# Kernel optimization log

Hardware: AMD Instinct MI355X
Metric: run time of the kernel (lower is better)

## Reference

```python
import jax, jax.numpy as jnp
import numpy as np

N_NODES = 100000
N_EDGES = 600000
D = 128
N_CLASSES = 16


def _degrees(idx, n):
    ones = jnp.ones(idx.shape[0], dtype=jnp.float32)
    return jax.ops.segment_sum(ones, idx, num_segments=n)


def graph_conv(src, dst, h, W, b):
    # DGL GraphConv, norm='both': D_out^{-1/2} A D_in^{-1/2} h W + b
    n = h.shape[0]
    deg_out = jnp.maximum(_degrees(src, n), 1.0)
    deg_in = jnp.maximum(_degrees(dst, n), 1.0)
    h = h * jax.lax.rsqrt(deg_out)[:, None]          # src-side norm
    h = h @ W                                         # dense transform
    msg = h[src]                                      # gather  [E, d]
    agg = jax.ops.segment_sum(msg, dst, num_segments=n)  # scatter-add
    agg = agg * jax.lax.rsqrt(deg_in)[:, None]        # dst-side norm
    return agg + b


def setup_inputs() -> dict:
    key = jax.random.key(0)
    ks = jax.random.split(key, 8)
    h = jax.random.normal(ks[0], (N_NODES, D), dtype=jnp.float32)
    src = jax.random.randint(ks[1], (N_EDGES,), 0, N_NODES)
    dst = jax.random.randint(ks[2], (N_EDGES,), 0, N_NODES)
    s = 1.0 / np.sqrt(D)
    W1 = jax.random.normal(ks[3], (D, D), dtype=jnp.float32) * s
    b1 = jnp.zeros((D,), dtype=jnp.float32)
    W2 = jax.random.normal(ks[4], (D, D), dtype=jnp.float32) * s
    b2 = jnp.zeros((D,), dtype=jnp.float32)
    Wc = jax.random.normal(ks[5], (D, N_CLASSES), dtype=jnp.float32) * s
    bc = jnp.zeros((N_CLASSES,), dtype=jnp.float32)
    return {"h": h, "src": src, "dst": dst, "W1": W1, "b1": b1,
            "W2": W2, "b2": b2, "Wc": Wc, "bc": bc}


def reference(h, src, dst, W1, b1, W2, b2, Wc, bc):
    h = jax.nn.relu(graph_conv(src, dst, h, W1, b1))
    h = jax.nn.relu(graph_conv(src, dst, h, W2, b2))
    return h @ Wc + bc
```

## Files before the change

kernel.cpp:

```cpp
#include <hip/hip_runtime.h>


typedef __attribute__((ext_vector_type(4))) _Float16 half4_t;
typedef __attribute__((ext_vector_type(16))) float floatx16;

__global__ __launch_bounds__(256) void scan1_kernel(
    const int* __restrict__ cntI, const int* __restrict__ cntO,
    int* __restrict__ excl, int* __restrict__ bsum,
    float* __restrict__ rs_out, float* __restrict__ rs_in, int n)
{
    __shared__ int tmp[256];
    int i = blockIdx.x * 256 + threadIdx.x;
    int v = 0;
    if (i < n) {
        v = cntI[i];
        rs_in[i]  = rsqrtf(fmaxf((float)v, 1.0f));
        rs_out[i] = rsqrtf(fmaxf((float)cntO[i], 1.0f));
    }
    tmp[threadIdx.x] = v;
    __syncthreads();
    for (int off = 1; off < 256; off <<= 1) {
        int t = (threadIdx.x >= off) ? tmp[threadIdx.x - off] : 0;
        __syncthreads();
        tmp[threadIdx.x] += t;
        __syncthreads();
    }
    if (i < n) excl[i] = tmp[threadIdx.x] - v;
    if (threadIdx.x == 255) bsum[blockIdx.x] = tmp[255];
}

__global__ __launch_bounds__(1024) void scan2_kernel(int* __restrict__ bsum, int nb)
{
    __shared__ int tmp[1024];
    int t = threadIdx.x;
    int v = (t < nb) ? bsum[t] : 0;
    tmp[t] = v;
    __syncthreads();
    for (int off = 1; off < 1024; off <<= 1) {
        int x = (t >= off) ? tmp[t - off] : 0;
        __syncthreads();
        tmp[t] += x;
        __syncthreads();
    }
    if (t < nb) bsum[t] = tmp[t] - v;
}

__global__ __launch_bounds__(256) void scan3_kernel(
    int* __restrict__ excl, const int* __restrict__ bsum, int n)
{
    int i = blockIdx.x * 256 + threadIdx.x;
    if (i < n) excl[i] += bsum[blockIdx.x];
}

__global__ __launch_bounds__(256) void fill_kernel(
    const int* __restrict__ src, const int* __restrict__ dst,
    const int* __restrict__ rank, const int* __restrict__ starts,
    int* __restrict__ eidx, int E)
{
    int e = blockIdx.x * blockDim.x + threadIdx.x;
    if (e < E) {
        eidx[starts[dst[e]] + rank[e]] = src[e];
    }
}

__global__ __launch_bounds__(256) void wpack_kernel(
    const float* __restrict__ W1, const float* __restrict__ W2,
    _Float16* __restrict__ WB1, _Float16* __restrict__ WB2)
{
    int gid = blockIdx.x * 256 + threadIdx.x;
    int j = gid & 16383;
    int i   = j & 3;
    int col = (j >> 2) & 127;
    int g   = (j >> 9) & 1;
    int kt  = j >> 10;
    int k = kt * 8 + g * 4 + i;
    if (gid < 16384) WB1[j] = (_Float16)W1[k * 128 + col];
    else             WB2[j] = (_Float16)W2[k * 128 + col];
}

__device__ __forceinline__ void mfma_and_store(
    char* xab, int bid, const _Float16* __restrict__ WB,
    _Float16* __restrict__ T, int n)
{
    const int tid  = threadIdx.x;
    const int lane = tid & 63;
    const int wv   = tid >> 6;
    const int m    = lane & 31;
    const int g    = lane >> 5;
    const int rhalf = wv & 1;
    const int chalf = wv >> 1;
    const int rbase = bid * 64 + rhalf * 32;

    floatx16 acc0 = {}, acc1 = {};
    const int arow = rhalf * 32 + m;
    const _Float16* wb = WB + (size_t)(g * 128 + chalf * 64 + m) * 4;

#pragma unroll 2
    for (int kt = 0; kt < 16; ++kt) {
        int cbyte = kt * 16 + g * 8;
        half4_t a = *(const half4_t*)(xab + ((arow * 256 + cbyte) ^ ((m & 7) << 4)));
        const _Float16* wk = wb + (size_t)kt * 1024;
        half4_t b0 = *(const half4_t*)(wk);
        half4_t b1 = *(const half4_t*)(wk + 128);
        acc0 = __builtin_amdgcn_mfma_f32_32x32x8f16(a, b0, acc0, 0, 0, 0);
        acc1 = __builtin_amdgcn_mfma_f32_32x32x8f16(a, b1, acc1, 0, 0, 0);
    }

#pragma unroll
    for (int rg = 0; rg < 16; ++rg) {
        int rd = (rg & 3) + 8 * (rg >> 2) + 4 * g;
        int orow = rbase + rd;
        if (orow < n) {
            _Float16* tp = T + (size_t)orow * 128 + chalf * 64 + m;
            tp[0]  = (_Float16)acc0[rg];
            tp[32] = (_Float16)acc1[rg];
        }
    }
}

__device__ __forceinline__ void gemm_tile64_f32in(
    int bid, const float* __restrict__ X, const _Float16* __restrict__ WB,
    _Float16* __restrict__ T, int n)
{
    __shared__ _Float16 xa[64 * 128];
    char* xab = (char*)xa;
    const int tid = threadIdx.x;
    {
        const int C = (tid & 31) * 4;
        const int rsub = tid >> 5;
#pragma unroll
        for (int p = 0; p < 8; ++p) {
            int R = p * 8 + rsub;
            int row = bid * 64 + R;
            half4_t a;
            if (row < n) {
                float4 v = *(const float4*)&X[(size_t)row * 128 + C];
                a[0] = (_Float16)v.x;
                a[1] = (_Float16)v.y;
                a[2] = (_Float16)v.z;
                a[3] = (_Float16)v.w;
            } else {
                a[0] = a[1] = a[2] = a[3] = (_Float16)0.f;
            }
            int byte = (R * 256 + C * 2) ^ ((R & 7) << 4);
            *(half4_t*)(xab + byte) = a;
        }
    }
    __syncthreads();
    mfma_and_store(xab, bid, WB, T, n);
}

__global__ __launch_bounds__(256) void fused1_kernel(
    const float* __restrict__ h, const _Float16* __restrict__ WB1,
    _Float16* __restrict__ T1,
    const int* __restrict__ src, const int* __restrict__ dst,
    int* __restrict__ cntO, int* __restrict__ cntI, int* __restrict__ rank,
    int n, int E, int GB, int S)
{
    int bid = blockIdx.x;
    int g = bid / S, r = bid - g * S;
    if (r == 0 && g < GB) {
        gemm_tile64_f32in(g, h, WB1, T1, n);
    } else {
        int ng = g + (r ? 1 : 0);
        if (ng > GB) ng = GB;
        int cb = bid - ng;
        int t = cb * 256 + threadIdx.x;
        if (t < E) {
            atomicAdd(&cntO[src[t]], 1);
        } else if (t < 2 * E) {
            int e = t - E;
            rank[e] = atomicAdd(&cntI[dst[e]], 1);
        }
    }
}

template <int PES>
__device__ __forceinline__ void edge_accum(
    const _Float16* __restrict__ T, const int* __restrict__ eidx,
    const float* __restrict__ rs_out, int s0, int s1, int t, float acc[4])
{
    int j = s0;
    for (; j + 7 < s1; j += 8) {
        int4 sA = *(const int4*)&eidx[j];
        int4 sB = *(const int4*)&eidx[j + 4];
        half4_t v0 = *(const half4_t*)&T[(size_t)sA.x * 128 + t * 4];
        half4_t v1 = *(const half4_t*)&T[(size_t)sA.y * 128 + t * 4];
        half4_t v2 = *(const half4_t*)&T[(size_t)sA.z * 128 + t * 4];
        half4_t v3 = *(const half4_t*)&T[(size_t)sA.w * 128 + t * 4];
        half4_t v4 = *(const half4_t*)&T[(size_t)sB.x * 128 + t * 4];
        half4_t v5 = *(const half4_t*)&T[(size_t)sB.y * 128 + t * 4];
        half4_t v6 = *(const half4_t*)&T[(size_t)sB.z * 128 + t * 4];
        half4_t v7 = *(const half4_t*)&T[(size_t)sB.w * 128 + t * 4];
        if (PES) {
            float r0 = rs_out[sA.x], r1 = rs_out[sA.y];
            float r2 = rs_out[sA.z], r3 = rs_out[sA.w];
            float r4 = rs_out[sB.x], r5 = rs_out[sB.y];
            float r6 = rs_out[sB.z], r7 = rs_out[sB.w];
#pragma unroll
            for (int i = 0; i < 4; ++i) {
                acc[i] = fmaf((float)v0[i], r0, acc[i]);
                acc[i] = fmaf((float)v1[i], r1, acc[i]);
                acc[i] = fmaf((float)v2[i], r2, acc[i]);
                acc[i] = fmaf((float)v3[i], r3, acc[i]);
                acc[i] = fmaf((float)v4[i], r4, acc[i]);
                acc[i] = fmaf((float)v5[i], r5, acc[i]);
                acc[i] = fmaf((float)v6[i], r6, acc[i]);
                acc[i] = fmaf((float)v7[i], r7, acc[i]);
            }
        } else {
#pragma unroll
            for (int i = 0; i < 4; ++i) {
                float s01 = (float)v0[i] + (float)v1[i];
                float s23 = (float)v2[i] + (float)v3[i];
                float s45 = (float)v4[i] + (float)v5[i];
                float s67 = (float)v6[i] + (float)v7[i];
                acc[i] += (s01 + s23) + (s45 + s67);
            }
        }
    }
    if (j + 3 < s1) {
        int4 sA = *(const int4*)&eidx[j];
        half4_t v0 = *(const half4_t*)&T[(size_t)sA.x * 128 + t * 4];
        half4_t v1 = *(const half4_t*)&T[(size_t)sA.y * 128 + t * 4];
        half4_t v2 = *(const half4_t*)&T[(size_t)sA.z * 128 + t * 4];
        half4_t v3 = *(const half4_t*)&T[(size_t)sA.w * 128 + t * 4];
        if (PES) {
            float r0 = rs_out[sA.x], r1 = rs_out[sA.y];
            float r2 = rs_out[sA.z], r3 = rs_out[sA.w];
#pragma unroll
            for (int i = 0; i < 4; ++i) {
                acc[i] = fmaf((float)v0[i], r0, acc[i]);
                acc[i] = fmaf((float)v1[i], r1, acc[i]);
                acc[i] = fmaf((float)v2[i], r2, acc[i]);
                acc[i] = fmaf((float)v3[i], r3, acc[i]);
            }
        } else {
#pragma unroll
            for (int i = 0; i < 4; ++i)
                acc[i] += ((float)v0[i] + (float)v1[i]) + ((float)v2[i] + (float)v3[i]);
        }
        j += 4;
    }
    for (; j < s1; ++j) {
        int sA = eidx[j];
        half4_t va = *(const half4_t*)&T[(size_t)sA * 128 + t * 4];
        float ra = PES ? rs_out[sA] : 1.0f;
#pragma unroll
        for (int i = 0; i < 4; ++i) acc[i] = fmaf((float)va[i], ra, acc[i]);
    }
}

__global__ __launch_bounds__(256) void g1g2_kernel(
    const _Float16* __restrict__ T1, const int* __restrict__ eidx,
    const int* __restrict__ starts, const float* __restrict__ rs_in,
    const float* __restrict__ rs_out, const float* __restrict__ bias,
    const _Float16* __restrict__ WB2, _Float16* __restrict__ T2, int n, int E)
{
    __shared__ _Float16 xa[64 * 128];
    char* xab = (char*)xa;
    const int tid = threadIdx.x;
    const int grp = tid >> 5;
    const int t   = tid & 31;
    const int bid = blockIdx.x;

#pragma unroll
    for (int it = 0; it < 8; ++it) {
        int R = grp * 8 + it;
        int node = bid * 64 + R;
        half4_t o;
        if (node < n) {
            int s0 = starts[node];
            int s1 = (node + 1 < n) ? starts[node + 1] : E;
            float acc[4] = {0.f, 0.f, 0.f, 0.f};
            edge_accum<1>(T1, eidx, rs_out, s0, s1, t, acc);
            float ri = rs_in[node];
            float ro = rs_out[node];
            float4 bv = *(const float4*)&bias[t * 4];
            float bb[4] = {bv.x, bv.y, bv.z, bv.w};
#pragma unroll
            for (int i = 0; i < 4; ++i)
                o[i] = (_Float16)(fmaxf(fmaf(acc[i], ri, bb[i]), 0.f) * ro);
        } else {
            o[0] = o[1] = o[2] = o[3] = (_Float16)0.f;
        }
        int byte = (R * 256 + t * 8) ^ ((R & 7) << 4);
        *(half4_t*)(xab + byte) = o;
    }
    __syncthreads();
    mfma_and_store(xab, bid, WB2, T2, n);
}

__global__ __launch_bounds__(256) void g2cls_kernel(
    const _Float16* __restrict__ T2, const int* __restrict__ eidx,
    const int* __restrict__ starts, const float* __restrict__ rs_in,
    const float* __restrict__ bias, const float* __restrict__ Wc,
    const float* __restrict__ bout, float* __restrict__ outp, int n, int E)
{
    __shared__ float wl[128 * 16];
    __shared__ _Float16 xs[16][128];
    const int tid = threadIdx.x;
    const int row0 = blockIdx.x * 16;
#pragma unroll
    for (int i0 = 0; i0 < 2; ++i0) {
        int i = tid + i0 * 256;
        ((float4*)wl)[i] = ((const float4*)Wc)[i];
    }

    const int grp = tid >> 5;
    const int t   = tid & 31;
#pragma unroll
    for (int it = 0; it < 2; ++it) {
        int r = grp * 2 + it;
        int node = row0 + r;
        half4_t o;
        if (node < n) {
            int s0 = starts[node];
            int s1 = (node + 1 < n) ? starts[node + 1] : E;
            float acc[4] = {0.f, 0.f, 0.f, 0.f};
            edge_accum<0>(T2, eidx, nullptr, s0, s1, t, acc);
            float ri = rs_in[node];
            float4 bv = *(const float4*)&bias[t * 4];
            float bb[4] = {bv.x, bv.y, bv.z, bv.w};
#pragma unroll
            for (int i = 0; i < 4; ++i)
                o[i] = (_Float16)fmaxf(fmaf(acc[i], ri, bb[i]), 0.f);
        } else {
            o[0] = o[1] = o[2] = o[3] = (_Float16)0.f;
        }
        *(half4_t*)&xs[r][t * 4] = o;
    }
    __syncthreads();

    int c = tid & 15, r = tid >> 4;
    float acc = 0.f;
#pragma unroll 4
    for (int k = 0; k < 128; k += 2) {
        float x0 = (float)xs[r][k];
        float x1 = (float)xs[r][k + 1];
        acc = fmaf(x0, wl[k * 16 + c], acc);
        acc = fmaf(x1, wl[(k + 1) * 16 + c], acc);
    }
    int row = row0 + r;
    if (row < n) outp[(size_t)row * 16 + c] = acc + bout[c];
}

extern "C" void kernel_launch(void* const* d_in, const int* in_sizes, int n_in,
                              void* d_out, int out_size, void* d_ws, size_t ws_size,
                              hipStream_t stream)
{
    const float* h   = (const float*)d_in[0];
    const int*   src = (const int*)d_in[1];
    const int*   dst = (const int*)d_in[2];
    const float* W1  = (const float*)d_in[3];
    const float* b1  = (const float*)d_in[4];
    const float* W2  = (const float*)d_in[5];
    const float* b2  = (const float*)d_in[6];
    const float* Wc  = (const float*)d_in[7];
    const float* bc  = (const float*)d_in[8];
    float* out = (float*)d_out;

    const int n = in_sizes[0] / 128;
    const int E = in_sizes[1];
    const int nb = (n + 255) / 256;

    char* ws = (char*)d_ws;
    int*   cntO    = (int*)ws;
    int*   cntI    = cntO + n;
    int*   rank    = cntI + n;
    float* rs_out  = (float*)(rank + E);
    float* rs_in   = rs_out + n;
    int*   starts  = (int*)(rs_in + n);
    int*   bsum    = starts + n;
    int*   eidx    = bsum + 1024;
    _Float16* WB1  = (_Float16*)(eidx + E);
    _Float16* WB2  = WB1 + 16384;
    size_t off = ((size_t)((char*)(WB2 + 16384) - ws) + 255) & ~(size_t)255;
    _Float16* bufA = (_Float16*)(ws + off);
    _Float16* bufB = bufA + (size_t)n * 128;

    const int CB = (2 * E + 255) / 256;
    const int GB = (n + 63) / 64;
    const int S  = (CB + GB) / GB;

    hipMemsetAsync(cntO, 0, (size_t)2 * n * sizeof(int), stream);
    wpack_kernel<<<128, 256, 0, stream>>>(W1, W2, WB1, WB2);
    fused1_kernel<<<CB + GB, 256, 0, stream>>>(h, WB1, bufA, src, dst,
                                               cntO, cntI, rank, n, E, GB, S);
    scan1_kernel<<<nb, 256, 0, stream>>>(cntI, cntO, starts, bsum, rs_out, rs_in, n);
    scan2_kernel<<<1, 1024, 0, stream>>>(bsum, nb);
    scan3_kernel<<<nb, 256, 0, stream>>>(starts, bsum, n);
    fill_kernel<<<(E + 255) / 256, 256, 0, stream>>>(src, dst, rank, starts, eidx, E);

    g1g2_kernel<<<GB, 256, 0, stream>>>(bufA, eidx, starts, rs_in, rs_out,
                                        b1, WB2, bufB, n, E);

    g2cls_kernel<<<(n + 15) / 16, 256, 0, stream>>>(bufB, eidx, starts, rs_in,
                                                    b2, Wc, bc, out, n, E);
}
```

Before: 193.2 us.

## Balance per-node aggregation with LDS work-stealing and fold memset into wpack

Replaces the static assignment of nodes to 32-lane groups in both aggregation kernels with a per-block shared-memory atomic counter. Each group grabs the next row dynamically, so groups that draw low-degree nodes pick up more rows instead of idling behind one heavy node. The separate hipMemsetAsync of the degree counters is removed and the zeroing is done inside the weight-packing kernel, saving one launch. The cost is an LDS atomic plus a shuffle per row, and unrolling across rows is no longer possible.

```diff
diff --git a/kernel.cpp b/kernel.cpp
--- a/kernel.cpp
+++ b/kernel.cpp
@@ -65,9 +65,11 @@
 
 __global__ __launch_bounds__(256) void wpack_kernel(
     const float* __restrict__ W1, const float* __restrict__ W2,
-    _Float16* __restrict__ WB1, _Float16* __restrict__ WB2)
+    _Float16* __restrict__ WB1, _Float16* __restrict__ WB2,
+    int* __restrict__ cnt, int n2)
 {
     int gid = blockIdx.x * 256 + threadIdx.x;
+    for (int i = gid; i < n2; i += 32768) cnt[i] = 0;
     int j = gid & 16383;
     int i   = j & 3;
     int col = (j >> 2) & 127;
@@ -258,16 +260,20 @@
     const _Float16* __restrict__ WB2, _Float16* __restrict__ T2, int n, int E)
 {
     __shared__ _Float16 xa[64 * 128];
+    __shared__ int pool;
     char* xab = (char*)xa;
     const int tid = threadIdx.x;
-    const int grp = tid >> 5;
+    if (tid == 0) pool = 0;
+    __syncthreads();
     const int t   = tid & 31;
     const int bid = blockIdx.x;
 
-#pragma unroll
-    for (int it = 0; it < 8; ++it) {
-        int R = grp * 8 + it;
-        int node = bid * 64 + R;
+    for (;;) {
+        int r = 0;
+        if (t == 0) r = atomicAdd(&pool, 1);
+        r = __shfl(r, 0, 32);
+        if (r >= 64) break;
+        int node = bid * 64 + r;
         half4_t o;
         if (node < n) {
             int s0 = starts[node];
@@ -284,7 +290,7 @@
         } else {
             o[0] = o[1] = o[2] = o[3] = (_Float16)0.f;
         }
-        int byte = (R * 256 + t * 8) ^ ((R & 7) << 4);
+        int byte = (r * 256 + t * 8) ^ ((r & 7) << 4);
         *(half4_t*)(xab + byte) = o;
     }
     __syncthreads();
@@ -299,19 +305,23 @@
 {
     __shared__ float wl[128 * 16];
     __shared__ _Float16 xs[16][128];
+    __shared__ int pool;
     const int tid = threadIdx.x;
     const int row0 = blockIdx.x * 16;
+    if (tid == 0) pool = 0;
 #pragma unroll
     for (int i0 = 0; i0 < 2; ++i0) {
         int i = tid + i0 * 256;
         ((float4*)wl)[i] = ((const float4*)Wc)[i];
     }
-
-    const int grp = tid >> 5;
-    const int t   = tid & 31;
-#pragma unroll
-    for (int it = 0; it < 2; ++it) {
-        int r = grp * 2 + it;
+    __syncthreads();
+
+    const int t = tid & 31;
+    for (;;) {
+        int r = 0;
+        if (t == 0) r = atomicAdd(&pool, 1);
+        r = __shfl(r, 0, 32);
+        if (r >= 16) break;
         int node = row0 + r;
         half4_t o;
         if (node < n) {
@@ -383,8 +393,7 @@
     const int GB = (n + 63) / 64;
     const int S  = (CB + GB) / GB;
 
-    hipMemsetAsync(cntO, 0, (size_t)2 * n * sizeof(int), stream);
-    wpack_kernel<<<128, 256, 0, stream>>>(W1, W2, WB1, WB2);
+    wpack_kernel<<<128, 256, 0, stream>>>(W1, W2, WB1, WB2, cntO, 2 * n);
     fused1_kernel<<<CB + GB, 256, 0, stream>>>(h, WB1, bufA, src, dst,
                                                cntO, cntI, rank, n, E, GB, S);
     scan1_kernel<<<nb, 256, 0, stream>>>(cntI, cntO, starts, bsum, rs_out, rs_in, n);
```

After: 195.4 us. No clear change (+1.1%).
